# Optimization experiments

Measured on AMD Instinct MI355X. Metric: run time of the kernel, lower is better.

Reference implementation:

```python
import jax, jax.numpy as jnp
import numpy as np

B, S, D = 1, 1024, 64
_EPS = 1e-15
_BND = 1.0 - 1e-7  # artanh domain clamp (mirrors geoopt projection)


def _sq(x):
    return jnp.sum(x * x, axis=-1, keepdims=True)


def _nrm(x):
    return jnp.sqrt(_sq(x) + _EPS)


def _normalize(x, axis, eps):
    n = jnp.sqrt(jnp.sum(x * x, axis=axis, keepdims=True))
    return x / jnp.maximum(n, eps)


def _mobius_add(x, y):
    x2, y2 = _sq(x), _sq(y)
    xy = jnp.sum(x * y, axis=-1, keepdims=True)
    num = (1.0 + 2.0 * xy + y2) * x + (1.0 - x2) * y
    den = 1.0 + 2.0 * xy + x2 * y2
    return num / jnp.maximum(den, _EPS)


def _expmap0(u):
    n = _nrm(u)
    return jnp.tanh(n) * u / n


def _logmap0(y):
    n = _nrm(y)
    return jnp.arctanh(jnp.clip(n, 0.0, _BND)) * y / n


def _dist(x, y):
    n = _nrm(_mobius_add(-x, y))[..., 0]
    return 2.0 * jnp.arctanh(jnp.clip(n, 0.0, _BND))


def _logmap(x, y):
    d = _mobius_add(-x, y)
    n = _nrm(d)
    lam = 2.0 / jnp.maximum(1.0 - _sq(x), _EPS)
    return (2.0 / lam) * jnp.arctanh(jnp.clip(n, 0.0, _BND)) * d / n


def _transp0back(x, v):
    return v / jnp.maximum(1.0 - _sq(x), _EPS)


def _forward(q_in, k_in, v_in, Wq, bq, Wk, bk, Wv, bv, Wo, bo,
             tau, gamma, tangent_scale, gumbel_u, v_rand_init):
    q = q_in @ Wq.T + bq
    k = k_in @ Wk.T + bk
    v = v_in @ Wv.T + bv

    q_hyp = _expmap0(q)   # [B,S,D]
    k_hyp = _expmap0(k)

    # all-pairs geodesic distances [B,S,S]
    dist = _dist(q_hyp[:, :, None, :], k_hyp[:, None, :, :])
    min_d = jnp.min(dist, axis=-1, keepdims=True)
    w_un = jnp.exp(-(dist - min_d))                         # unnormalized weights
    w_sum = jnp.sum(w_un, axis=-1, keepdims=True) + 1e-8
    w_probs = w_un / w_sum
    h = jnp.einsum('bqk,bkd->bqd', w_probs, v)

    # Einstein midpoint: weighted Euclidean centroid of pre-map keys -> manifold
    centroid_euc = jnp.einsum('bqk,bkd->bqd', w_un / w_sum, k)
    centroid_hyp = _expmap0(centroid_euc)                   # [B,S,D]

    c2k = _dist(centroid_hyp[:, :, None, :], k_hyp[:, None, :, :])  # [B,S,S]
    wnv = w_un / w_sum
    entropy = -jnp.sum(wnv * jnp.log(wnv + 1e-8), axis=-1, keepdims=True)
    eff_mass = jnp.exp(entropy)
    variance = jnp.sum(wnv * c2k ** 2, axis=-1, keepdims=True)
    tension = variance - tau * eff_mass                     # [B,S,1]

    # matrix-free TPCA power iteration on weighted local tangents
    k_local = _logmap(centroid_hyp[:, :, None, :], k_hyp[:, None, :, :])  # [B,S,S,D]
    weighted_k = k_local * jnp.sqrt(w_un[..., None] + 1e-8)
    v_r = _normalize(v_rand_init, axis=2, eps=1e-12)        # [B,S,D,1]
    for _ in range(3):
        proj = jnp.einsum('bqkd,bqdo->bqko', weighted_k, v_r)
        v_r = jnp.einsum('bqkd,bqko->bqdo', weighted_k, proj)
        v_r = _normalize(v_r, axis=2, eps=1e-12)
    w_proj_local = v_r[..., 0]                              # [B,S,D]
    w_proj_global = _transp0back(centroid_hyp, w_proj_local)

    q_tan = _logmap0(q_hyp)
    c_tan = _logmap0(centroid_hyp)
    fallback = _normalize(q_tan - c_tan, axis=-1, eps=1e-8)
    w_proj = jnp.where(variance > 1e-5, w_proj_global, fallback)

    h_norm = _nrm(h)
    h_comp = jnp.arcsinh(h_norm) * (h / (h_norm + 1e-8))

    # Pitchfork bifurcation (c = 1)
    x = jnp.sum(h_comp * w_proj, axis=-1, keepdims=True)
    diss = (tension > 0).astype(h.dtype)
    h_mag = _nrm(h_comp)
    amplitude = h_mag * jnp.tanh(tension) * diss
    g = -jnp.log(-jnp.log(gumbel_u))                        # gumbel noise, logits = 0
    y_soft = jax.nn.softmax(g / 0.5, axis=-1)
    y_hard = jax.nn.one_hot(jnp.argmax(y_soft, axis=-1), 2, dtype=h.dtype)
    gp = y_soft + jax.lax.stop_gradient(y_hard - y_soft)    # straight-through
    eps_g = (gp[..., 0] - gp[..., 1])[..., None]            # gp @ [1,-1]
    x_star = eps_g * amplitude
    delta_c = jnp.tanh(x_star - x)
    h_prime = h_comp + delta_c * w_proj
    hp_norm = _nrm(h_prime) + 1e-8
    h_pb = h_prime * (jnp.tanh(hp_norm * tangent_scale) / hp_norm)
    h_prime_hyp = _expmap0(h_pb)

    h_out_bif = _logmap0(h_prime_hyp)
    gate = jax.nn.sigmoid(gamma)
    h_fused = (1.0 - gate) * h + gate * h_out_bif
    return h_fused @ Wo.T + bo


def setup_inputs() -> dict:
    key = jax.random.key(0)
    ks = jax.random.split(key, 10)
    std = 0.02
    return {
        'q_in': jax.random.normal(ks[0], (B, S, D), jnp.float32),
        'k_in': jax.random.normal(ks[1], (B, S, D), jnp.float32),
        'v_in': jax.random.normal(ks[2], (B, S, D), jnp.float32),
        'Wq': std * jax.random.normal(ks[3], (D, D), jnp.float32),
        'bq': jnp.zeros((D,), jnp.float32),
        'Wk': std * jax.random.normal(ks[4], (D, D), jnp.float32),
        'bk': jnp.zeros((D,), jnp.float32),
        'Wv': std * jax.random.normal(ks[5], (D, D), jnp.float32),
        'bv': jnp.zeros((D,), jnp.float32),
        'Wo': std * jax.random.normal(ks[6], (D, D), jnp.float32),
        'bo': jnp.zeros((D,), jnp.float32),
        'tau': jnp.float32(5.0),
        'gamma': jnp.float32(0.0),
        'tangent_scale': jnp.float32(0.1),
        'gumbel_u': jax.random.uniform(ks[7], (B, S, 2), jnp.float32, 1e-6, 1.0 - 1e-6),
        'v_rand_init': jax.random.normal(ks[8], (B, S, D, 1), jnp.float32),
    }


def reference(q_in, k_in, v_in, Wq, bq, Wk, bk, Wv, bv, Wo, bo,
              tau, gamma, tangent_scale, gumbel_u, v_rand_init):
    return _forward(q_in, k_in, v_in, Wq, bq, Wk, bk, Wv, bv, Wo, bo,
                    tau, gamma, tangent_scale, gumbel_u, v_rand_init)
```

## Files before the change

kernel.cpp:

```cpp
#include <hip/hip_runtime.h>
#include <math.h>

#define S 1024
#define D 64
#define BND 0.99999994f
#define FINF 3.4e38f
#define C4(v,c) ((&(v).x)[c])

__device__ __forceinline__ float waveSum(float v){
  #pragma unroll
  for(int o=32;o>0;o>>=1) v += __shfl_xor(v,o,64);
  return v;
}
__device__ __forceinline__ float waveMin(float v){
  #pragma unroll
  for(int o=32;o>0;o>>=1) v = fminf(v,__shfl_xor(v,o,64));
  return v;
}
__device__ __forceinline__ float blockSum512(float v, float* red){
  float w = waveSum(v);
  int wid = threadIdx.x>>6;
  __syncthreads();
  if((threadIdx.x&63)==0) red[wid]=w;
  __syncthreads();
  float s=0.f;
  #pragma unroll
  for(int k=0;k<8;k++) s+=red[k];
  return s;
}
__device__ __forceinline__ float blockMin512(float v, float* red){
  float w = waveMin(v);
  int wid = threadIdx.x>>6;
  __syncthreads();
  if((threadIdx.x&63)==0) red[wid]=w;
  __syncthreads();
  float s=red[0];
  #pragma unroll
  for(int k=1;k<8;k++) s=fminf(s,red[k]);
  return s;
}
__device__ __forceinline__ float4 mk4(const float* a){
  float4 r; r.x=a[0]; r.y=a[1]; r.z=a[2]; r.w=a[3]; return r;
}

__global__ __launch_bounds__(64) void k_proj(
  const float* __restrict__ qin, const float* __restrict__ kin, const float* __restrict__ vin,
  const float* __restrict__ Wq, const float* __restrict__ bq,
  const float* __restrict__ Wk, const float* __restrict__ bk,
  const float* __restrict__ Wv, const float* __restrict__ bv,
  const float* __restrict__ vrand,
  float* __restrict__ q_hyp, float* __restrict__ k_hyp, float* __restrict__ kT,
  float* __restrict__ vproj, float* __restrict__ kproj,
  float* __restrict__ q2, float* __restrict__ k2, float* __restrict__ v_r)
{
  const int i = blockIdx.x, d = threadIdx.x;
  __shared__ __align__(16) float lq[D], lk[D], lv[D];
  lq[d]=qin[i*D+d]; lk[d]=kin[i*D+d]; lv[d]=vin[i*D+d];
  __syncthreads();
  float aq=bq[d], ak=bk[d], av=bv[d];
  const float4* wq4=(const float4*)(Wq + d*D);
  const float4* wk4=(const float4*)(Wk + d*D);
  const float4* wv4=(const float4*)(Wv + d*D);
  #pragma unroll
  for(int e=0;e<16;e++){
    float4 a=wq4[e], b=wk4[e], c=wv4[e];
    aq += lq[4*e]*a.x + lq[4*e+1]*a.y + lq[4*e+2]*a.z + lq[4*e+3]*a.w;
    ak += lk[4*e]*b.x + lk[4*e+1]*b.y + lk[4*e+2]*b.z + lk[4*e+3]*b.w;
    av += lv[4*e]*c.x + lv[4*e+1]*c.y + lv[4*e+2]*c.z + lv[4*e+3]*c.w;
  }
  float nq = sqrtf(waveSum(aq*aq)+1e-15f);
  float qh = tanhf(nq)*aq/nq;
  q_hyp[i*D+d]=qh;
  float q2v = waveSum(qh*qh);
  if(d==0) q2[i]=q2v;
  float nk = sqrtf(waveSum(ak*ak)+1e-15f);
  float kh = tanhf(nk)*ak/nk;
  k_hyp[i*D+d]=kh;
  kT[(size_t)d*S + i]=kh;
  float k2v = waveSum(kh*kh);
  if(d==0) k2[i]=k2v;
  vproj[i*D+d]=av;
  kproj[i*D+d]=ak;
  float vr = vrand[i*D+d];
  float nn = sqrtf(waveSum(vr*vr));
  v_r[i*D+d] = vr/fmaxf(nn,1e-12f);
}

__global__ __launch_bounds__(512,4) void k_wc(
  const float* __restrict__ q_hyp, const float* __restrict__ kT,
  const float* __restrict__ q2a, const float* __restrict__ k2a,
  const float* __restrict__ vproj, const float* __restrict__ kproj,
  float* __restrict__ wbuf, float* __restrict__ wsum, float* __restrict__ effm,
  float* __restrict__ h, float* __restrict__ c_hyp, float* __restrict__ c2)
{
  const int i0=blockIdx.x*2, tid=threadIdx.x;
  __shared__ __align__(16) float qv[2][D];
  __shared__ __align__(16) float wl[2][S];
  __shared__ __align__(16) float4 sA[1024];
  __shared__ __align__(16) float4 sB[1024];
  __shared__ float red[8];
  if(tid<128) qv[tid>>6][tid&63]=q_hyp[i0*D+tid];
  __syncthreads();
  const float x20=q2a[i0], x21=q2a[i0+1];
  const float B0=1.f-x20, B1=1.f-x21;
  const int jf=tid&255, dh=tid>>8;
  const float4* kT4=(const float4*)kT;
  {
    float4 p0={0,0,0,0}, p1={0,0,0,0};
    #pragma unroll 8
    for(int dd=0; dd<32; ++dd){
      const int d=(dh<<5)+dd;
      const float4 y=kT4[d*256+jf];
      const float c0=qv[0][d], c1=qv[1][d];
      p0.x+=c0*y.x; p0.y+=c0*y.y; p0.z+=c0*y.z; p0.w+=c0*y.w;
      p1.x+=c1*y.x; p1.y+=c1*y.y; p1.z+=c1*y.z; p1.w+=c1*y.w;
    }
    sA[(dh*2+0)*256+jf]=p0;
    sA[(dh*2+1)*256+jf]=p1;
  }
  __syncthreads();
  float dist[2][4];
  float mn0=FINF, mn1=FINF;
  if(tid<256){
    const float4 qa=sA[jf], qb=sA[512+jf];
    const float4 ra=sA[256+jf], rb=sA[768+jf];
    const float4 y2v=((const float4*)k2a)[jf];
    #pragma unroll
    for(int c=0;c<4;c++){
      const float y2=C4(y2v,c);
      {
        const float dot=C4(qa,c)+C4(qb,c);
        const float A=1.f-2.f*dot+y2;
        const float den=fmaxf(1.f-2.f*dot+x20*y2,1e-15f);
        const float num2=fmaxf(A*A*x20 + B0*B0*y2 - 2.f*A*B0*dot, 0.f);
        const float nn=sqrtf(num2/(den*den)+1e-15f);
        dist[0][c]=2.f*atanhf(fminf(nn,BND));
        mn0=fminf(mn0,dist[0][c]);
      }
      {
        const float dot=C4(ra,c)+C4(rb,c);
        const float A=1.f-2.f*dot+y2;
        const float den=fmaxf(1.f-2.f*dot+x21*y2,1e-15f);
        const float num2=fmaxf(A*A*x21 + B1*B1*y2 - 2.f*A*B1*dot, 0.f);
        const float nn=sqrtf(num2/(den*den)+1e-15f);
        dist[1][c]=2.f*atanhf(fminf(nn,BND));
        mn1=fminf(mn1,dist[1][c]);
      }
    }
  }
  const float m0=blockMin512(mn0,red);
  const float m1=blockMin512(mn1,red);
  float s0=0.f, s1=0.f;
  float w0c[4], w1c[4];
  if(tid<256){
    #pragma unroll
    for(int c=0;c<4;c++){
      w0c[c]=expf(m0-dist[0][c]); s0+=w0c[c];
      w1c[c]=expf(m1-dist[1][c]); s1+=w1c[c];
    }
    ((float4*)&wl[0][0])[jf]=mk4(w0c);
    ((float4*)&wl[1][0])[jf]=mk4(w1c);
    ((float4*)(wbuf+(size_t)i0*S))[jf]=mk4(w0c);
    ((float4*)(wbuf+(size_t)(i0+1)*S))[jf]=mk4(w1c);
  }
  s0=blockSum512(s0,red)+1e-8f;
  s1=blockSum512(s1,red)+1e-8f;
  if(tid==0){ wsum[i0]=s0; wsum[i0+1]=s1; }
  const float inv0=1.f/s0, inv1=1.f/s1;
  float e0=0.f, e1=0.f;
  if(tid<256){
    #pragma unroll
    for(int c=0;c<4;c++){
      const float p0=w0c[c]*inv0; e0 -= p0*logf(p0+1e-8f);
      const float p1=w1c[c]*inv1; e1 -= p1*logf(p1+1e-8f);
    }
  }
  e0=blockSum512(e0,red);
  e1=blockSum512(e1,red);
  if(tid==0){ effm[i0]=expf(e0); effm[i0+1]=expf(e1); }
  const int dq=tid&15, g=tid>>4;
  float4 ah0={0,0,0,0}, ah1={0,0,0,0}, ac0={0,0,0,0}, ac1={0,0,0,0};
  #pragma unroll 4
  for(int jj=0;jj<32;jj++){
    const int j=jj*32+g;
    const float4 yv=((const float4*)(vproj + j*D))[dq];
    const float4 yk=((const float4*)(kproj + j*D))[dq];
    const float u0=wl[0][j], u1=wl[1][j];
    ah0.x+=u0*yv.x; ah0.y+=u0*yv.y; ah0.z+=u0*yv.z; ah0.w+=u0*yv.w;
    ah1.x+=u1*yv.x; ah1.y+=u1*yv.y; ah1.z+=u1*yv.z; ah1.w+=u1*yv.w;
    ac0.x+=u0*yk.x; ac0.y+=u0*yk.y; ac0.z+=u0*yk.z; ac0.w+=u0*yk.w;
    ac1.x+=u1*yk.x; ac1.y+=u1*yk.y; ac1.z+=u1*yk.z; ac1.w+=u1*yk.w;
  }
  float* pA=(float*)sA;
  float* pB=(float*)sB;
  *(float4*)&pA[(g*2+0)*64+dq*4]=ah0;
  *(float4*)&pA[(g*2+1)*64+dq*4]=ah1;
  *(float4*)&pB[(g*2+0)*64+dq*4]=ac0;
  *(float4*)&pB[(g*2+1)*64+dq*4]=ac1;
  __syncthreads();
  if(tid<128){
    const int q=tid>>6, d=tid&63;
    float hs=0.f, cs=0.f;
    #pragma unroll 8
    for(int gg=0;gg<32;gg++){ hs+=pA[(gg*2+q)*64+d]; cs+=pB[(gg*2+q)*64+d]; }
    const float invq = q ? inv1 : inv0;
    h[(i0+q)*D+d]=hs*invq;
    const float ca=cs*invq;
    const float n=sqrtf(waveSum(ca*ca)+1e-15f);
    const float ch=tanhf(n)*ca/n;
    c_hyp[(i0+q)*D+d]=ch;
    const float c2v=waveSum(ch*ch);
    if(d==0) c2[i0+q]=c2v;
  }
}

__global__ __launch_bounds__(512,4) void k_pmega(
  const float* __restrict__ c_hyp, const float* __restrict__ k_hyp,
  const float* __restrict__ kT,
  const float* __restrict__ c2a, const float* __restrict__ k2a,
  const float* __restrict__ wbuf, const float* __restrict__ wsum,
  const float* __restrict__ effm, const float* __restrict__ tau_p,
  const float* __restrict__ h, const float* __restrict__ q_hyp,
  const float* __restrict__ q2a, const float* __restrict__ v_r,
  const float* __restrict__ gu, const float* __restrict__ gamma_p,
  const float* __restrict__ ts_p, const float* __restrict__ Wo,
  const float* __restrict__ bo, float* __restrict__ out)
{
  const int i0=blockIdx.x*2, tid=threadIdx.x;
  __shared__ __align__(16) float cv[2][D];
  __shared__ __align__(16) float vv[2][D];
  __shared__ __align__(16) float aal[2][S];
  __shared__ __align__(16) float bbl[2][S];
  __shared__ __align__(16) float prow[2][S];
  __shared__ __align__(16) float4 sA[1024];
  __shared__ __align__(16) float fus[2][D];
  __shared__ float red[8];
  __shared__ float scal[2][4];

  if(tid<128){ cv[tid>>6][tid&63]=c_hyp[i0*D+tid]; vv[tid>>6][tid&63]=v_r[i0*D+tid]; }
  __syncthreads();
  const float x20=c2a[i0], x21=c2a[i0+1];
  const float Bc0=1.f-x20, Bc1=1.f-x21;
  const float mB0=fmaxf(Bc0,1e-15f), mB1=fmaxf(Bc1,1e-15f);
  const float inv0=1.f/wsum[i0], inv1=1.f/wsum[i0+1];
  const int jf=tid&255, dh=tid>>8;
  const float4* kT4=(const float4*)kT;

  {
    float4 p0={0,0,0,0}, p1={0,0,0,0};
    #pragma unroll 8
    for(int dd=0; dd<32; ++dd){
      const int d=(dh<<5)+dd;
      const float4 y=kT4[d*256+jf];
      const float c0=cv[0][d], c1=cv[1][d];
      p0.x+=c0*y.x; p0.y+=c0*y.y; p0.z+=c0*y.z; p0.w+=c0*y.w;
      p1.x+=c1*y.x; p1.y+=c1*y.y; p1.z+=c1*y.z; p1.w+=c1*y.w;
    }
    sA[(dh*2+0)*256+jf]=p0;
    sA[(dh*2+1)*256+jf]=p1;
  }
  __syncthreads();
  float var0p=0.f, var1p=0.f;
  if(tid<256){
    const float4 qa=sA[jf], qb=sA[512+jf];
    const float4 ra=sA[256+jf], rb=sA[768+jf];
    const float4 y2v=((const float4*)k2a)[jf];
    const float4 w0v=((const float4*)(wbuf+(size_t)i0*S))[jf];
    const float4 w1v=((const float4*)(wbuf+(size_t)(i0+1)*S))[jf];
    float a0c[4],b0c[4],a1c[4],b1c[4];
    #pragma unroll
    for(int c=0;c<4;c++){
      const float y2=C4(y2v,c);
      {
        const float dot=C4(qa,c)+C4(qb,c);
        const float A=1.f-2.f*dot+y2;
        const float den=fmaxf(1.f-2.f*dot+x20*y2,1e-15f);
        const float num2=fmaxf(A*A*x20+Bc0*Bc0*y2-2.f*A*Bc0*dot,0.f);
        const float nn=sqrtf(num2/(den*den)+1e-15f);
        const float art=atanhf(fminf(nn,BND));
        const float w=C4(w0v,c);
        var0p += w*inv0*4.f*art*art;
        const float coef=sqrtf(w+1e-8f)*mB0*art/(nn*den);
        a0c[c]=-coef*A; b0c[c]=coef*Bc0;
      }
      {
        const float dot=C4(ra,c)+C4(rb,c);
        const float A=1.f-2.f*dot+y2;
        const float den=fmaxf(1.f-2.f*dot+x21*y2,1e-15f);
        const float num2=fmaxf(A*A*x21+Bc1*Bc1*y2-2.f*A*Bc1*dot,0.f);
        const float nn=sqrtf(num2/(den*den)+1e-15f);
        const float art=atanhf(fminf(nn,BND));
        const float w=C4(w1v,c);
        var1p += w*inv1*4.f*art*art;
        const float coef=sqrtf(w+1e-8f)*mB1*art/(nn*den);
        a1c[c]=-coef*A; b1c[c]=coef*Bc1;
      }
    }
    ((float4*)&aal[0][0])[jf]=mk4(a0c);
    ((float4*)&aal[1][0])[jf]=mk4(a1c);
    ((float4*)&bbl[0][0])[jf]=mk4(b0c);
    ((float4*)&bbl[1][0])[jf]=mk4(b1c);
  }
  const float var0=blockSum512(var0p,red);
  const float var1=blockSum512(var1p,red);
  if(tid==0){
    scal[0][0]=var0; scal[0][1]=var0 - tau_p[0]*effm[i0];
    scal[1][0]=var1; scal[1][1]=var1 - tau_p[0]*effm[i0+1];
  }

  const int dq=tid&15, g=tid>>4;
  for(int it=0; it<3; ++it){
    __syncthreads();
    if(tid<128){
      const int q=tid>>6, d=tid&63;
      const float cd=waveSum(cv[q][d]*vv[q][d]);
      if(d==0) scal[q][2]=cd;
    }
    __syncthreads();
    const float cdot0=scal[0][2], cdot1=scal[1][2];
    {
      float4 p0={0,0,0,0}, p1={0,0,0,0};
      #pragma unroll 8
      for(int dd=0; dd<32; ++dd){
        const int d=(dh<<5)+dd;
        const float4 y=kT4[d*256+jf];
        const float c0=vv[0][d], c1=vv[1][d];
        p0.x+=c0*y.x; p0.y+=c0*y.y; p0.z+=c0*y.z; p0.w+=c0*y.w;
        p1.x+=c1*y.x; p1.y+=c1*y.y; p1.z+=c1*y.z; p1.w+=c1*y.w;
      }
      sA[(dh*2+0)*256+jf]=p0;
      sA[(dh*2+1)*256+jf]=p1;
    }
    __syncthreads();
    float sal0p=0.f, sal1p=0.f;
    if(tid<256){
      const float4 qa=sA[jf], qb=sA[512+jf];
      const float4 ra=sA[256+jf], rb=sA[768+jf];
      const float4 av0=((float4*)&aal[0][0])[jf];
      const float4 av1=((float4*)&aal[1][0])[jf];
      const float4 bv0=((float4*)&bbl[0][0])[jf];
      const float4 bv1=((float4*)&bbl[1][0])[jf];
      float pr0[4], pr1[4];
      #pragma unroll
      for(int c=0;c<4;c++){
        const float t0=C4(qa,c)+C4(qb,c);
        const float t1=C4(ra,c)+C4(rb,c);
        const float p0=C4(av0,c)*cdot0 + C4(bv0,c)*t0;
        const float p1=C4(av1,c)*cdot1 + C4(bv1,c)*t1;
        pr0[c]=p0*C4(bv0,c); sal0p += p0*C4(av0,c);
        pr1[c]=p1*C4(bv1,c); sal1p += p1*C4(av1,c);
      }
      ((float4*)&prow[0][0])[jf]=mk4(pr0);
      ((float4*)&prow[1][0])[jf]=mk4(pr1);
    }
    const float sal0=blockSum512(sal0p,red);
    const float sal1=blockSum512(sal1p,red);
    float4 a0={0,0,0,0}, a1={0,0,0,0};
    #pragma unroll 4
    for(int jj=0;jj<32;jj++){
      const int j=jj*32+g;
      const float4 y=((const float4*)(k_hyp + j*D))[dq];
      const float u0=prow[0][j], u1=prow[1][j];
      a0.x+=u0*y.x; a0.y+=u0*y.y; a0.z+=u0*y.z; a0.w+=u0*y.w;
      a1.x+=u1*y.x; a1.y+=u1*y.y; a1.z+=u1*y.z; a1.w+=u1*y.w;
    }
    float* pA=(float*)sA;
    *(float4*)&pA[(g*2+0)*64+dq*4]=a0;
    *(float4*)&pA[(g*2+1)*64+dq*4]=a1;
    __syncthreads();
    if(tid<128){
      const int q=tid>>6, d=tid&63;
      float od=(q?sal1:sal0)*cv[q][d];
      #pragma unroll 8
      for(int gg=0;gg<32;gg++) od += pA[(gg*2+q)*64+d];
      const float nn=sqrtf(waveSum(od*od));
      vv[q][d]=od/fmaxf(nn,1e-12f);
    }
  }
  __syncthreads();

  if(tid<128){
    const int q=tid>>6, d=tid&63;
    const int i=i0+q;
    const float x2q = q ? x21 : x20;
    const float vd=vv[q][d];
    const float vars=scal[q][0], tns=scal[q][1];
    const float hd=h[i*D+d];
    const float qd=q_hyp[i*D+d];
    const float q2=q2a[i];
    const float wpg=vd/fmaxf(1.f-x2q,1e-15f);
    const float nq=sqrtf(q2+1e-15f);
    const float qt=atanhf(fminf(nq,BND))*qd/nq;
    const float ncn=sqrtf(x2q+1e-15f);
    const float ct=atanhf(fminf(ncn,BND))*cv[q][d]/ncn;
    const float df=qt-ct;
    const float nd=sqrtf(waveSum(df*df));
    const float fb=df/fmaxf(nd,1e-8f);
    const float wp=(vars>1e-5f)?wpg:fb;
    const float hn=sqrtf(waveSum(hd*hd)+1e-15f);
    const float hc=asinhf(hn)*hd/(hn+1e-8f);
    const float x=waveSum(hc*wp);
    const float hmag=sqrtf(waveSum(hc*hc)+1e-15f);
    const float amp=(tns>0.f)? hmag*tanhf(tns) : 0.f;
    const float u0=gu[i*2], u1=gu[i*2+1];
    const float eg=(u0>=u1)?1.f:-1.f;
    const float dc=tanhf(eg*amp - x);
    const float hp=hc+dc*wp;
    const float hpn=sqrtf(waveSum(hp*hp)+1e-15f)+1e-8f;
    const float hpb=hp*(tanhf(hpn*ts_p[0])/hpn);
    const float n2=sqrtf(waveSum(hpb*hpb)+1e-15f);
    const float hyp=tanhf(n2)*hpb/n2;
    const float n3=sqrtf(waveSum(hyp*hyp)+1e-15f);
    const float bif=atanhf(fminf(n3,BND))*hyp/n3;
    const float gate=1.f/(1.f+expf(-gamma_p[0]));
    fus[q][d]=(1.f-gate)*hd + gate*bif;
  }
  __syncthreads();
  if(tid<128){
    const int q=tid>>6, d=tid&63;
    float acc=bo[d];
    const float4* wo4=(const float4*)(Wo + d*D);
    #pragma unroll
    for(int e=0;e<16;e++){
      float4 wv=wo4[e];
      acc += fus[q][4*e]*wv.x + fus[q][4*e+1]*wv.y + fus[q][4*e+2]*wv.z + fus[q][4*e+3]*wv.w;
    }
    out[(i0+q)*D+d]=acc;
  }
}

extern "C" void kernel_launch(void* const* d_in, const int* in_sizes, int n_in,
                              void* d_out, int out_size, void* d_ws, size_t ws_size,
                              hipStream_t stream)
{
  const float* qin=(const float*)d_in[0];
  const float* kin=(const float*)d_in[1];
  const float* vin=(const float*)d_in[2];
  const float* Wq=(const float*)d_in[3];
  const float* bq=(const float*)d_in[4];
  const float* Wk=(const float*)d_in[5];
  const float* bk=(const float*)d_in[6];
  const float* Wv=(const float*)d_in[7];
  const float* bv=(const float*)d_in[8];
  const float* Wo=(const float*)d_in[9];
  const float* bo=(const float*)d_in[10];
  const float* tau=(const float*)d_in[11];
  const float* gamma=(const float*)d_in[12];
  const float* tscale=(const float*)d_in[13];
  const float* gu=(const float*)d_in[14];
  const float* vrand=(const float*)d_in[15];
  float* out=(float*)d_out;

  float* p=(float*)d_ws;
  float* q_hyp=p; p+=S*D;
  float* k_hyp=p; p+=S*D;
  float* kT=p;    p+=S*D;
  float* vproj=p; p+=S*D;
  float* kproj=p; p+=S*D;
  float* v_r=p;   p+=S*D;
  float* h=p;     p+=S*D;
  float* c_hyp=p; p+=S*D;
  float* q2=p;   p+=S;
  float* k2=p;   p+=S;
  float* c2=p;   p+=S;
  float* wsum=p; p+=S;
  float* effm=p; p+=S;
  float* wbuf=p; p+=(size_t)S*S;

  k_proj<<<S,64,0,stream>>>(qin,kin,vin,Wq,bq,Wk,bk,Wv,bv,vrand,
                            q_hyp,k_hyp,kT,vproj,kproj,q2,k2,v_r);
  k_wc<<<S/2,512,0,stream>>>(q_hyp,kT,q2,k2,vproj,kproj,
                             wbuf,wsum,effm,h,c_hyp,c2);
  k_pmega<<<S/2,512,0,stream>>>(c_hyp,k_hyp,kT,c2,k2,wbuf,wsum,effm,tau,
                                h,q_hyp,q2,v_r,gu,gamma,tscale,Wo,bo,out);
}
```

Measured before the change: 79.04 us.

## Use half-precision transposed keys in power iteration and restructure distance passes

Adds a packed fp16 copy of the transposed hyperbolic keys and reads it in the three power-iteration matvecs, which halves the bytes loaded there. The distance passes now give each thread two keys across all 64 dims, so the split-dim shared-memory reduction and one barrier go away and all 512 threads take part in the distance math. The paired min and sum reductions are merged into float2 block reductions, and the c·v dot product is folded into the normalisation step. The fp16 keys cost precision in the iterated eigenvector direction.

```diff
diff --git a/kernel.cpp b/kernel.cpp
--- a/kernel.cpp
+++ b/kernel.cpp
@@ -1,46 +1,48 @@
 #include <hip/hip_runtime.h>
+#include <hip/hip_fp16.h>
 #include <math.h>
 
 #define S 1024
 #define D 64
 #define BND 0.99999994f
 #define FINF 3.4e38f
-#define C4(v,c) ((&(v).x)[c])
+#define FMA4(acc,s,v) { (acc).x+=(s)*(v).x; (acc).y+=(s)*(v).y; (acc).z+=(s)*(v).z; (acc).w+=(s)*(v).w; }
 
 __device__ __forceinline__ float waveSum(float v){
   #pragma unroll
   for(int o=32;o>0;o>>=1) v += __shfl_xor(v,o,64);
   return v;
 }
-__device__ __forceinline__ float waveMin(float v){
-  #pragma unroll
-  for(int o=32;o>0;o>>=1) v = fminf(v,__shfl_xor(v,o,64));
-  return v;
-}
-__device__ __forceinline__ float blockSum512(float v, float* red){
-  float w = waveSum(v);
-  int wid = threadIdx.x>>6;
-  __syncthreads();
-  if((threadIdx.x&63)==0) red[wid]=w;
-  __syncthreads();
-  float s=0.f;
-  #pragma unroll
-  for(int k=0;k<8;k++) s+=red[k];
+__device__ __forceinline__ float2 blockSum512_v2(float2 v, float* red){
+  #pragma unroll
+  for(int o=32;o>0;o>>=1){ v.x+=__shfl_xor(v.x,o,64); v.y+=__shfl_xor(v.y,o,64); }
+  const int wid=threadIdx.x>>6;
+  __syncthreads();
+  if((threadIdx.x&63)==0){ red[wid*2]=v.x; red[wid*2+1]=v.y; }
+  __syncthreads();
+  float2 s={0.f,0.f};
+  #pragma unroll
+  for(int k=0;k<8;k++){ s.x+=red[k*2]; s.y+=red[k*2+1]; }
   return s;
 }
-__device__ __forceinline__ float blockMin512(float v, float* red){
-  float w = waveMin(v);
-  int wid = threadIdx.x>>6;
-  __syncthreads();
-  if((threadIdx.x&63)==0) red[wid]=w;
-  __syncthreads();
-  float s=red[0];
-  #pragma unroll
-  for(int k=1;k<8;k++) s=fminf(s,red[k]);
+__device__ __forceinline__ float2 blockMin512_v2(float2 v, float* red){
+  #pragma unroll
+  for(int o=32;o>0;o>>=1){ v.x=fminf(v.x,__shfl_xor(v.x,o,64)); v.y=fminf(v.y,__shfl_xor(v.y,o,64)); }
+  const int wid=threadIdx.x>>6;
+  __syncthreads();
+  if((threadIdx.x&63)==0){ red[wid*2]=v.x; red[wid*2+1]=v.y; }
+  __syncthreads();
+  float2 s={red[0],red[1]};
+  #pragma unroll
+  for(int k=1;k<8;k++){ s.x=fminf(s.x,red[k*2]); s.y=fminf(s.y,red[k*2+1]); }
   return s;
 }
-__device__ __forceinline__ float4 mk4(const float* a){
-  float4 r; r.x=a[0]; r.y=a[1]; r.z=a[2]; r.w=a[3]; return r;
+__device__ __forceinline__ float distF(float dot, float y2, float x2, float B){
+  const float A=1.f-2.f*dot+y2;
+  const float den=fmaxf(1.f-2.f*dot+x2*y2,1e-15f);
+  const float num2=fmaxf(A*A*x2 + B*B*y2 - 2.f*A*B*dot, 0.f);
+  const float nn=sqrtf(num2/(den*den)+1e-15f);
+  return 2.f*atanhf(fminf(nn,BND));
 }
 
 __global__ __launch_bounds__(64) void k_proj(
@@ -50,11 +52,13 @@
   const float* __restrict__ Wv, const float* __restrict__ bv,
   const float* __restrict__ vrand,
   float* __restrict__ q_hyp, float* __restrict__ k_hyp, float* __restrict__ kT,
+  __half* __restrict__ kTp,
   float* __restrict__ vproj, float* __restrict__ kproj,
   float* __restrict__ q2, float* __restrict__ k2, float* __restrict__ v_r)
 {
   const int i = blockIdx.x, d = threadIdx.x;
   __shared__ __align__(16) float lq[D], lk[D], lv[D];
+  __shared__ __align__(16) float skh[D];
   lq[d]=qin[i*D+d]; lk[d]=kin[i*D+d]; lv[d]=vin[i*D+d];
   __syncthreads();
   float aq=bq[d], ak=bk[d], av=bv[d];
@@ -77,6 +81,7 @@
   float kh = tanhf(nk)*ak/nk;
   k_hyp[i*D+d]=kh;
   kT[(size_t)d*S + i]=kh;
+  skh[d]=kh;
   float k2v = waveSum(kh*kh);
   if(d==0) k2[i]=k2v;
   vproj[i*D+d]=av;
@@ -84,6 +89,11 @@
   float vr = vrand[i*D+d];
   float nn = sqrtf(waveSum(vr*vr));
   v_r[i*D+d] = vr/fmaxf(nn,1e-12f);
+  __syncthreads();
+  if(d<32){
+    __half2 hp=__floats2half2_rn(skh[2*d], skh[2*d+1]);
+    ((__half2*)kTp)[(size_t)d*S + i]=hp;
+  }
 }
 
 __global__ __launch_bounds__(512,4) void k_wc(
@@ -98,105 +108,59 @@
   __shared__ __align__(16) float wl[2][S];
   __shared__ __align__(16) float4 sA[1024];
   __shared__ __align__(16) float4 sB[1024];
-  __shared__ float red[8];
+  __shared__ float red[16];
   if(tid<128) qv[tid>>6][tid&63]=q_hyp[i0*D+tid];
   __syncthreads();
   const float x20=q2a[i0], x21=q2a[i0+1];
   const float B0=1.f-x20, B1=1.f-x21;
-  const int jf=tid&255, dh=tid>>8;
-  const float4* kT4=(const float4*)kT;
-  {
-    float4 p0={0,0,0,0}, p1={0,0,0,0};
-    #pragma unroll 8
-    for(int dd=0; dd<32; ++dd){
-      const int d=(dh<<5)+dd;
-      const float4 y=kT4[d*256+jf];
-      const float c0=qv[0][d], c1=qv[1][d];
-      p0.x+=c0*y.x; p0.y+=c0*y.y; p0.z+=c0*y.z; p0.w+=c0*y.w;
-      p1.x+=c1*y.x; p1.y+=c1*y.y; p1.z+=c1*y.z; p1.w+=c1*y.w;
-    }
-    sA[(dh*2+0)*256+jf]=p0;
-    sA[(dh*2+1)*256+jf]=p1;
-  }
-  __syncthreads();
-  float dist[2][4];
-  float mn0=FINF, mn1=FINF;
-  if(tid<256){
-    const float4 qa=sA[jf], qb=sA[512+jf];
-    const float4 ra=sA[256+jf], rb=sA[768+jf];
-    const float4 y2v=((const float4*)k2a)[jf];
-    #pragma unroll
-    for(int c=0;c<4;c++){
-      const float y2=C4(y2v,c);
-      {
-        const float dot=C4(qa,c)+C4(qb,c);
-        const float A=1.f-2.f*dot+y2;
-        const float den=fmaxf(1.f-2.f*dot+x20*y2,1e-15f);
-        const float num2=fmaxf(A*A*x20 + B0*B0*y2 - 2.f*A*B0*dot, 0.f);
-        const float nn=sqrtf(num2/(den*den)+1e-15f);
-        dist[0][c]=2.f*atanhf(fminf(nn,BND));
-        mn0=fminf(mn0,dist[0][c]);
-      }
-      {
-        const float dot=C4(ra,c)+C4(rb,c);
-        const float A=1.f-2.f*dot+y2;
-        const float den=fmaxf(1.f-2.f*dot+x21*y2,1e-15f);
-        const float num2=fmaxf(A*A*x21 + B1*B1*y2 - 2.f*A*B1*dot, 0.f);
-        const float nn=sqrtf(num2/(den*den)+1e-15f);
-        dist[1][c]=2.f*atanhf(fminf(nn,BND));
-        mn1=fminf(mn1,dist[1][c]);
-      }
-    }
-  }
-  const float m0=blockMin512(mn0,red);
-  const float m1=blockMin512(mn1,red);
-  float s0=0.f, s1=0.f;
-  float w0c[4], w1c[4];
-  if(tid<256){
-    #pragma unroll
-    for(int c=0;c<4;c++){
-      w0c[c]=expf(m0-dist[0][c]); s0+=w0c[c];
-      w1c[c]=expf(m1-dist[1][c]); s1+=w1c[c];
-    }
-    ((float4*)&wl[0][0])[jf]=mk4(w0c);
-    ((float4*)&wl[1][0])[jf]=mk4(w1c);
-    ((float4*)(wbuf+(size_t)i0*S))[jf]=mk4(w0c);
-    ((float4*)(wbuf+(size_t)(i0+1)*S))[jf]=mk4(w1c);
-  }
-  s0=blockSum512(s0,red)+1e-8f;
-  s1=blockSum512(s1,red)+1e-8f;
+  const int j0=2*tid;
+  float t00=0.f,t01=0.f,t10=0.f,t11=0.f;
+  #pragma unroll 8
+  for(int d=0;d<64;++d){
+    const float2 y=*(const float2*)(kT + (size_t)d*S + j0);
+    const float c0=qv[0][d], c1=qv[1][d];
+    t00+=y.x*c0; t01+=y.x*c1; t10+=y.y*c0; t11+=y.y*c1;
+  }
+  const float2 y2p=*(const float2*)(k2a + j0);
+  const float ds00=distF(t00,y2p.x,x20,B0);
+  const float ds10=distF(t10,y2p.y,x20,B0);
+  const float ds01=distF(t01,y2p.x,x21,B1);
+  const float ds11=distF(t11,y2p.y,x21,B1);
+  float2 mn2={fminf(ds00,ds10), fminf(ds01,ds11)};
+  mn2=blockMin512_v2(mn2,red);
+  const float w00=expf(mn2.x-ds00), w10=expf(mn2.x-ds10);
+  const float w01=expf(mn2.y-ds01), w11=expf(mn2.y-ds11);
+  { float2 a={w00,w10}; *(float2*)&wl[0][j0]=a; *(float2*)(wbuf+(size_t)i0*S+j0)=a; }
+  { float2 a={w01,w11}; *(float2*)&wl[1][j0]=a; *(float2*)(wbuf+(size_t)(i0+1)*S+j0)=a; }
+  float2 s2={w00+w10, w01+w11};
+  s2=blockSum512_v2(s2,red);
+  const float s0=s2.x+1e-8f, s1=s2.y+1e-8f;
   if(tid==0){ wsum[i0]=s0; wsum[i0+1]=s1; }
   const float inv0=1.f/s0, inv1=1.f/s1;
-  float e0=0.f, e1=0.f;
-  if(tid<256){
-    #pragma unroll
-    for(int c=0;c<4;c++){
-      const float p0=w0c[c]*inv0; e0 -= p0*logf(p0+1e-8f);
-      const float p1=w1c[c]*inv1; e1 -= p1*logf(p1+1e-8f);
-    }
-  }
-  e0=blockSum512(e0,red);
-  e1=blockSum512(e1,red);
-  if(tid==0){ effm[i0]=expf(e0); effm[i0+1]=expf(e1); }
+  float2 e2={0.f,0.f};
+  { const float p0=w00*inv0, p1=w10*inv0; e2.x -= p0*logf(p0+1e-8f)+p1*logf(p1+1e-8f); }
+  { const float p0=w01*inv1, p1=w11*inv1; e2.y -= p0*logf(p0+1e-8f)+p1*logf(p1+1e-8f); }
+  e2=blockSum512_v2(e2,red);
+  if(tid==0){ effm[i0]=expf(e2.x); effm[i0+1]=expf(e2.y); }
   const int dq=tid&15, g=tid>>4;
-  float4 ah0={0,0,0,0}, ah1={0,0,0,0}, ac0={0,0,0,0}, ac1={0,0,0,0};
-  #pragma unroll 4
-  for(int jj=0;jj<32;jj++){
-    const int j=jj*32+g;
-    const float4 yv=((const float4*)(vproj + j*D))[dq];
-    const float4 yk=((const float4*)(kproj + j*D))[dq];
-    const float u0=wl[0][j], u1=wl[1][j];
-    ah0.x+=u0*yv.x; ah0.y+=u0*yv.y; ah0.z+=u0*yv.z; ah0.w+=u0*yv.w;
-    ah1.x+=u1*yv.x; ah1.y+=u1*yv.y; ah1.z+=u1*yv.z; ah1.w+=u1*yv.w;
-    ac0.x+=u0*yk.x; ac0.y+=u0*yk.y; ac0.z+=u0*yk.z; ac0.w+=u0*yk.w;
-    ac1.x+=u1*yk.x; ac1.y+=u1*yk.y; ac1.z+=u1*yk.z; ac1.w+=u1*yk.w;
-  }
-  float* pA=(float*)sA;
-  float* pB=(float*)sB;
-  *(float4*)&pA[(g*2+0)*64+dq*4]=ah0;
-  *(float4*)&pA[(g*2+1)*64+dq*4]=ah1;
-  *(float4*)&pB[(g*2+0)*64+dq*4]=ac0;
-  *(float4*)&pB[(g*2+1)*64+dq*4]=ac1;
+  float* const pA=(float*)sA;
+  float* const pB=(float*)sB;
+  {
+    float4 ah0={0,0,0,0}, ah1={0,0,0,0}, ac0={0,0,0,0}, ac1={0,0,0,0};
+    #pragma unroll 4
+    for(int jj=0;jj<32;jj++){
+      const int j=jj*32+g;
+      const float4 yv=((const float4*)(vproj + j*D))[dq];
+      const float4 yk=((const float4*)(kproj + j*D))[dq];
+      const float u0=wl[0][j], u1=wl[1][j];
+      FMA4(ah0,u0,yv); FMA4(ah1,u1,yv);
+      FMA4(ac0,u0,yk); FMA4(ac1,u1,yk);
+    }
+    *(float4*)&pA[(g*2+0)*64+dq*4]=ah0;
+    *(float4*)&pA[(g*2+1)*64+dq*4]=ah1;
+    *(float4*)&pB[(g*2+0)*64+dq*4]=ac0;
+    *(float4*)&pB[(g*2+1)*64+dq*4]=ac1;
+  }
   __syncthreads();
   if(tid<128){
     const int q=tid>>6, d=tid&63;
@@ -216,7 +180,7 @@
 
 __global__ __launch_bounds__(512,4) void k_pmega(
   const float* __restrict__ c_hyp, const float* __restrict__ k_hyp,
-  const float* __restrict__ kT,
+  const float* __restrict__ kT, const __half* __restrict__ kTp,
   const float* __restrict__ c2a, const float* __restrict__ k2a,
   const float* __restrict__ wbuf, const float* __restrict__ wsum,
   const float* __restrict__ effm, const float* __restrict__ tau_p,
@@ -234,169 +198,162 @@
   __shared__ __align__(16) float prow[2][S];
   __shared__ __align__(16) float4 sA[1024];
   __shared__ __align__(16) float fus[2][D];
-  __shared__ float red[8];
-  __shared__ float scal[2][4];
-
-  if(tid<128){ cv[tid>>6][tid&63]=c_hyp[i0*D+tid]; vv[tid>>6][tid&63]=v_r[i0*D+tid]; }
+  __shared__ float red[16];
+  __shared__ float scd[2];
+  float* const pA=(float*)sA;
+
+  if(tid<128){
+    const int q=tid>>6, d=tid&63;
+    const float ch=c_hyp[i0*D+tid];
+    const float vr=v_r[i0*D+tid];
+    cv[q][d]=ch; vv[q][d]=vr;
+    const float cd=waveSum(ch*vr);
+    if(d==0) scd[q]=cd;
+  }
   __syncthreads();
   const float x20=c2a[i0], x21=c2a[i0+1];
   const float Bc0=1.f-x20, Bc1=1.f-x21;
   const float mB0=fmaxf(Bc0,1e-15f), mB1=fmaxf(Bc1,1e-15f);
   const float inv0=1.f/wsum[i0], inv1=1.f/wsum[i0+1];
-  const int jf=tid&255, dh=tid>>8;
-  const float4* kT4=(const float4*)kT;
-
+  const int j0=2*tid;
+  const int dq=tid&15, g=tid>>4;
+  const float tau=tau_p[0];
+
+  float2 var2;
   {
-    float4 p0={0,0,0,0}, p1={0,0,0,0};
+    float u00=0.f,u01=0.f,u10=0.f,u11=0.f;
     #pragma unroll 8
-    for(int dd=0; dd<32; ++dd){
-      const int d=(dh<<5)+dd;
-      const float4 y=kT4[d*256+jf];
+    for(int d=0;d<64;++d){
+      const float2 y=*(const float2*)(kT + (size_t)d*S + j0);
       const float c0=cv[0][d], c1=cv[1][d];
-      p0.x+=c0*y.x; p0.y+=c0*y.y; p0.z+=c0*y.z; p0.w+=c0*y.w;
-      p1.x+=c1*y.x; p1.y+=c1*y.y; p1.z+=c1*y.z; p1.w+=c1*y.w;
-    }
-    sA[(dh*2+0)*256+jf]=p0;
-    sA[(dh*2+1)*256+jf]=p1;
-  }
-  __syncthreads();
-  float var0p=0.f, var1p=0.f;
-  if(tid<256){
-    const float4 qa=sA[jf], qb=sA[512+jf];
-    const float4 ra=sA[256+jf], rb=sA[768+jf];
-    const float4 y2v=((const float4*)k2a)[jf];
-    const float4 w0v=((const float4*)(wbuf+(size_t)i0*S))[jf];
-    const float4 w1v=((const float4*)(wbuf+(size_t)(i0+1)*S))[jf];
-    float a0c[4],b0c[4],a1c[4],b1c[4];
-    #pragma unroll
-    for(int c=0;c<4;c++){
-      const float y2=C4(y2v,c);
-      {
-        const float dot=C4(qa,c)+C4(qb,c);
-        const float A=1.f-2.f*dot+y2;
-        const float den=fmaxf(1.f-2.f*dot+x20*y2,1e-15f);
-        const float num2=fmaxf(A*A*x20+Bc0*Bc0*y2-2.f*A*Bc0*dot,0.f);
-        const float nn=sqrtf(num2/(den*den)+1e-15f);
-        const float art=atanhf(fminf(nn,BND));
-        const float w=C4(w0v,c);
-        var0p += w*inv0*4.f*art*art;
-        const float coef=sqrtf(w+1e-8f)*mB0*art/(nn*den);
-        a0c[c]=-coef*A; b0c[c]=coef*Bc0;
+      u00+=y.x*c0; u01+=y.x*c1; u10+=y.y*c0; u11+=y.y*c1;
+    }
+    const float2 y2p=*(const float2*)(k2a + j0);
+    const float2 w0=*(const float2*)(wbuf+(size_t)i0*S+j0);
+    const float2 w1=*(const float2*)(wbuf+(size_t)(i0+1)*S+j0);
+    float var0=0.f, var1=0.f;
+    float a00,a10,a01,a11,b00,b10,b01,b11;
+    {
+      const float A=1.f-2.f*u00+y2p.x;
+      const float den=fmaxf(1.f-2.f*u00+x20*y2p.x,1e-15f);
+      const float num2=fmaxf(A*A*x20+Bc0*Bc0*y2p.x-2.f*A*Bc0*u00,0.f);
+      const float nn=sqrtf(num2/(den*den)+1e-15f);
+      const float art=atanhf(fminf(nn,BND));
+      var0 += w0.x*inv0*4.f*art*art;
+      const float coef=sqrtf(w0.x+1e-8f)*mB0*art/(nn*den);
+      a00=-coef*A; b00=coef*Bc0;
+    }
+    {
+      const float A=1.f-2.f*u10+y2p.y;
+      const float den=fmaxf(1.f-2.f*u10+x20*y2p.y,1e-15f);
+      const float num2=fmaxf(A*A*x20+Bc0*Bc0*y2p.y-2.f*A*Bc0*u10,0.f);
+      const float nn=sqrtf(num2/(den*den)+1e-15f);
+      const float art=atanhf(fminf(nn,BND));
+      var0 += w0.y*inv0*4.f*art*art;
+      const float coef=sqrtf(w0.y+1e-8f)*mB0*art/(nn*den);
+      a10=-coef*A; b10=coef*Bc0;
+    }
+    {
+      const float A=1.f-2.f*u01+y2p.x;
+      const float den=fmaxf(1.f-2.f*u01+x21*y2p.x,1e-15f);
+      const float num2=fmaxf(A*A*x21+Bc1*Bc1*y2p.x-2.f*A*Bc1*u01,0.f);
+      const float nn=sqrtf(num2/(den*den)+1e-15f);
+      const float art=atanhf(fminf(nn,BND));
+      var1 += w1.x*inv1*4.f*art*art;
+      const float coef=sqrtf(w1.x+1e-8f)*mB1*art/(nn*den);
+      a01=-coef*A; b01=coef*Bc1;
+    }
+    {
+      const float A=1.f-2.f*u11+y2p.y;
+      const float den=fmaxf(1.f-2.f*u11+x21*y2p.y,1e-15f);
+      const float num2=fmaxf(A*A*x21+Bc1*Bc1*y2p.y-2.f*A*Bc1*u11,0.f);
+      const float nn=sqrtf(num2/(den*den)+1e-15f);
+      const float art=atanhf(fminf(nn,BND));
+      var1 += w1.y*inv1*4.f*art*art;
+      const float coef=sqrtf(w1.y+1e-8f)*mB1*art/(nn*den);
+      a11=-coef*A; b11=coef*Bc1;
+    }
+    { float2 t={a00,a10}; *(float2*)&aal[0][j0]=t; }
+    { float2 t={a01,a11}; *(float2*)&aal[1][j0]=t; }
+    { float2 t={b00,b10}; *(float2*)&bbl[0][j0]=t; }
+    { float2 t={b01,b11}; *(float2*)&bbl[1][j0]=t; }
+    float2 v2={var0,var1};
+    var2=blockSum512_v2(v2,red);
+  }
+
+  float2 sal2;
+  for(int it3=0; it3<3; ++it3){
+    float t00=0.f,t01=0.f,t10=0.f,t11=0.f;
+    #pragma unroll 8
+    for(int dp=0;dp<32;++dp){
+      const __half2 h0=((const __half2*)kTp)[(size_t)dp*S + j0];
+      const __half2 h1=((const __half2*)kTp)[(size_t)dp*S + j0+1];
+      const float2 f0=__half22float2(h0);
+      const float2 f1=__half22float2(h1);
+      const float2 v0=*(const float2*)&vv[0][2*dp];
+      const float2 v1=*(const float2*)&vv[1][2*dp];
+      t00 += f0.x*v0.x + f0.y*v0.y;
+      t01 += f0.x*v1.x + f0.y*v1.y;
+      t10 += f1.x*v0.x + f1.y*v0.y;
+      t11 += f1.x*v1.x + f1.y*v1.y;
+    }
+    {
+      const float cd0=scd[0], cd1=scd[1];
+      const float2 a0=*(const float2*)&aal[0][j0], b0=*(const float2*)&bbl[0][j0];
+      const float2 a1=*(const float2*)&aal[1][j0], b1=*(const float2*)&bbl[1][j0];
+      const float p00=a0.x*cd0+b0.x*t00, p10=a0.y*cd0+b0.y*t10;
+      const float p01=a1.x*cd1+b1.x*t01, p11=a1.y*cd1+b1.y*t11;
+      { float2 t={p00*b0.x, p10*b0.y}; *(float2*)&prow[0][j0]=t; }
+      { float2 t={p01*b1.x, p11*b1.y}; *(float2*)&prow[1][j0]=t; }
+      float2 s={p00*a0.x+p10*a0.y, p01*a1.x+p11*a1.y};
+      sal2=blockSum512_v2(s,red);
+    }
+    {
+      float4 a0={0,0,0,0}, a1={0,0,0,0};
+      #pragma unroll 4
+      for(int jj=0;jj<32;jj++){
+        const int j=jj*32+g;
+        const float4 y=((const float4*)(k_hyp + j*D))[dq];
+        const float u0=prow[0][j], u1=prow[1][j];
+        FMA4(a0,u0,y); FMA4(a1,u1,y);
       }
-      {
-        const float dot=C4(ra,c)+C4(rb,c);
-        const float A=1.f-2.f*dot+y2;
-        const float den=fmaxf(1.f-2.f*dot+x21*y2,1e-15f);
-        const float num2=fmaxf(A*A*x21+Bc1*Bc1*y2-2.f*A*Bc1*dot,0.f);
-        const float nn=sqrtf(num2/(den*den)+1e-15f);
-        const float art=atanhf(fminf(nn,BND));
-        const float w=C4(w1v,c);
-        var1p += w*inv1*4.f*art*art;
-        const float coef=sqrtf(w+1e-8f)*mB1*art/(nn*den);
-        a1c[c]=-coef*A; b1c[c]=coef*Bc1;
-      }
-    }
-    ((float4*)&aal[0][0])[jf]=mk4(a0c);
-    ((float4*)&aal[1][0])[jf]=mk4(a1c);
-    ((float4*)&bbl[0][0])[jf]=mk4(b0c);
-    ((float4*)&bbl[1][0])[jf]=mk4(b1c);
-  }
-  const float var0=blockSum512(var0p,red);
-  const float var1=blockSum512(var1p,red);
-  if(tid==0){
-    scal[0][0]=var0; scal[0][1]=var0 - tau_p[0]*effm[i0];
-    scal[1][0]=var1; scal[1][1]=var1 - tau_p[0]*effm[i0+1];
-  }
-
-  const int dq=tid&15, g=tid>>4;
-  for(int it=0; it<3; ++it){
+      *(float4*)&pA[(g*2+0)*64+dq*4]=a0;
+      *(float4*)&pA[(g*2+1)*64+dq*4]=a1;
+    }
     __syncthreads();
     if(tid<128){
       const int q=tid>>6, d=tid&63;
-      const float cd=waveSum(cv[q][d]*vv[q][d]);
-      if(d==0) scal[q][2]=cd;
-    }
-    __syncthreads();
-    const float cdot0=scal[0][2], cdot1=scal[1][2];
-    {
-      float4 p0={0,0,0,0}, p1={0,0,0,0};
-      #pragma unroll 8
-      for(int dd=0; dd<32; ++dd){
-        const int d=(dh<<5)+dd;
-        const float4 y=kT4[d*256+jf];
-        const float c0=vv[0][d], c1=vv[1][d];
-        p0.x+=c0*y.x; p0.y+=c0*y.y; p0.z+=c0*y.z; p0.w+=c0*y.w;
-        p1.x+=c1*y.x; p1.y+=c1*y.y; p1.z+=c1*y.z; p1.w+=c1*y.w;
-      }
-      sA[(dh*2+0)*256+jf]=p0;
-      sA[(dh*2+1)*256+jf]=p1;
-    }
-    __syncthreads();
-    float sal0p=0.f, sal1p=0.f;
-    if(tid<256){
-      const float4 qa=sA[jf], qb=sA[512+jf];
-      const float4 ra=sA[256+jf], rb=sA[768+jf];
-      const float4 av0=((float4*)&aal[0][0])[jf];
-      const float4 av1=((float4*)&aal[1][0])[jf];
-      const float4 bv0=((float4*)&bbl[0][0])[jf];
-      const float4 bv1=((float4*)&bbl[1][0])[jf];
-      float pr0[4], pr1[4];
-      #pragma unroll
-      for(int c=0;c<4;c++){
-        const float t0=C4(qa,c)+C4(qb,c);
-        const float t1=C4(ra,c)+C4(rb,c);
-        const float p0=C4(av0,c)*cdot0 + C4(bv0,c)*t0;
-        const float p1=C4(av1,c)*cdot1 + C4(bv1,c)*t1;
-        pr0[c]=p0*C4(bv0,c); sal0p += p0*C4(av0,c);
-        pr1[c]=p1*C4(bv1,c); sal1p += p1*C4(av1,c);
-      }
-      ((float4*)&prow[0][0])[jf]=mk4(pr0);
-      ((float4*)&prow[1][0])[jf]=mk4(pr1);
-    }
-    const float sal0=blockSum512(sal0p,red);
-    const float sal1=blockSum512(sal1p,red);
-    float4 a0={0,0,0,0}, a1={0,0,0,0};
-    #pragma unroll 4
-    for(int jj=0;jj<32;jj++){
-      const int j=jj*32+g;
-      const float4 y=((const float4*)(k_hyp + j*D))[dq];
-      const float u0=prow[0][j], u1=prow[1][j];
-      a0.x+=u0*y.x; a0.y+=u0*y.y; a0.z+=u0*y.z; a0.w+=u0*y.w;
-      a1.x+=u1*y.x; a1.y+=u1*y.y; a1.z+=u1*y.z; a1.w+=u1*y.w;
-    }
-    float* pA=(float*)sA;
-    *(float4*)&pA[(g*2+0)*64+dq*4]=a0;
-    *(float4*)&pA[(g*2+1)*64+dq*4]=a1;
-    __syncthreads();
-    if(tid<128){
-      const int q=tid>>6, d=tid&63;
-      float od=(q?sal1:sal0)*cv[q][d];
+      float od=(q?sal2.y:sal2.x)*cv[q][d];
       #pragma unroll 8
       for(int gg=0;gg<32;gg++) od += pA[(gg*2+q)*64+d];
       const float nn=sqrtf(waveSum(od*od));
-      vv[q][d]=od/fmaxf(nn,1e-12f);
-    }
-  }
-  __syncthreads();
+      const float vn=od/fmaxf(nn,1e-12f);
+      vv[q][d]=vn;
+      const float cd=waveSum(cv[q][d]*vn);
+      if(d==0) scd[q]=cd;
+    }
+    __syncthreads();
+  }
 
   if(tid<128){
     const int q=tid>>6, d=tid&63;
     const int i=i0+q;
-    const float x2q = q ? x21 : x20;
+    const float vart = q ? var2.y : var2.x;
+    const float tns = vart - tau*effm[i];
+    const float x2q_c = q ? x21 : x20;
     const float vd=vv[q][d];
-    const float vars=scal[q][0], tns=scal[q][1];
     const float hd=h[i*D+d];
     const float qd=q_hyp[i*D+d];
     const float q2=q2a[i];
-    const float wpg=vd/fmaxf(1.f-x2q,1e-15f);
+    const float wpg=vd/fmaxf(1.f-x2q_c,1e-15f);
     const float nq=sqrtf(q2+1e-15f);
     const float qt=atanhf(fminf(nq,BND))*qd/nq;
-    const float ncn=sqrtf(x2q+1e-15f);
+    const float ncn=sqrtf(x2q_c+1e-15f);
     const float ct=atanhf(fminf(ncn,BND))*cv[q][d]/ncn;
     const float df=qt-ct;
     const float nd=sqrtf(waveSum(df*df));
     const float fb=df/fmaxf(nd,1e-8f);
-    const float wp=(vars>1e-5f)?wpg:fb;
+    const float wp=(vart>1e-5f)?wpg:fb;
     const float hn=sqrtf(waveSum(hd*hd)+1e-15f);
     const float hc=asinhf(hn)*hd/(hn+1e-8f);
     const float x=waveSum(hc*wp);
@@ -465,12 +422,13 @@
   float* c2=p;   p+=S;
   float* wsum=p; p+=S;
   float* effm=p; p+=S;
+  __half* kTp=(__half*)p; p+=(S*D)/2;
   float* wbuf=p; p+=(size_t)S*S;
 
   k_proj<<<S,64,0,stream>>>(qin,kin,vin,Wq,bq,Wk,bk,Wv,bv,vrand,
-                            q_hyp,k_hyp,kT,vproj,kproj,q2,k2,v_r);
+                            q_hyp,k_hyp,kT,kTp,vproj,kproj,q2,k2,v_r);
   k_wc<<<S/2,512,0,stream>>>(q_hyp,kT,q2,k2,vproj,kproj,
                              wbuf,wsum,effm,h,c_hyp,c2);
-  k_pmega<<<S/2,512,0,stream>>>(c_hyp,k_hyp,kT,c2,k2,wbuf,wsum,effm,tau,
+  k_pmega<<<S/2,512,0,stream>>>(c_hyp,k_hyp,kT,kTp,c2,k2,wbuf,wsum,effm,tau,
                                 h,q_hyp,q2,v_r,gu,gamma,tscale,Wo,bo,out);
 }
```

After: 82.55 us. 4.4% more time.
